# Kernel optimization log

Hardware: AMD Instinct MI355X
Metric: run time of the kernel (lower is better)

## Reference

```python
import math
import jax, jax.numpy as jnp
import numpy as np

B, H, W, CP = 64, 512, 512, 400
HALF_X = W // 2          # int, matches width//2 in the original
HALF_Y = H / 2.0         # float, matches height/2 in the original
NPTS = CP // 2
PI = math.pi


def fix_radians(tt):
    # Faithful translation of: -relu(-(2pi - relu(-tt)), threshold=-2pi) + relu(tt)
    inner = -(2.0 * PI - jnp.maximum(-tt, 0.0))
    thr = jnp.where(inner > -2.0 * PI, inner, 0.0)  # keras relu with threshold=-2pi
    return -thr + jnp.maximum(tt, 0.0)


def half_contour(pred_norm):
    # pred_norm: [B, H, W] in [0, 1]
    pred1st = jnp.round(pred_norm[:, :, :HALF_X])          # [B, H, W/2]
    x1st = jnp.sum(pred1st, axis=2)                        # [B, H] column count per row
    xaux = jnp.clip(x1st, 0.0, 1.0)                        # relu(.., threshold=0, max_value=1)
    ythtop = HALF_Y - jnp.sum(xaux[:, :HALF_X], axis=1)    # [B]
    ythbottom = HALF_Y + jnp.sum(xaux[:, HALF_X:], axis=1) # [B]
    rows = jnp.arange(W, dtype=pred_norm.dtype)[None, :]   # [1, W] (H == W assumed by original)
    # relu(rows - top) + top == max(rows, top); then min with bottom
    y1st = jnp.minimum(jnp.maximum(rows, ythtop[:, None]), ythbottom[:, None])  # [B, W]
    # Original: x1st <- half_x - x1st, then cart2pol(x1st - half_x, y1st - half_y)
    xc = -x1st                                             # [B, H]
    yc = y1st - HALF_Y                                     # [B, W]
    r1st = jnp.sqrt(xc ** 2 + yc ** 2)                     # [B, H]
    tt1st = fix_radians(jnp.arctan2(yc, xc))               # [B, H]

    tt_new = (PI / 2.0) + jnp.arange(NPTS, dtype=pred_norm.dtype) * (PI / NPTS)  # [NPTS]

    # RBF angular smoothing (get_rbf_points), with periodic wraparound copies
    tt_1 = jnp.concatenate([tt1st - 2.0 * PI, tt1st, tt1st + 2.0 * PI], axis=1)  # [B, 3H]
    r_cat = jnp.concatenate([r1st, r1st, r1st], axis=1)                          # [B, 3H]
    d2 = (tt_1[:, :, None] - tt_new[None, None, :]) ** 2                         # [B, 3H, NPTS]
    d2 = jnp.minimum(d2, 1.0)
    wgt = jnp.exp(-100.0 * d2)                                                   # [B, 3H, NPTS]
    wgt = wgt / jnp.sum(wgt, axis=1, keepdims=True)
    r_new = jnp.einsum('bkn,bk->bn', wgt, r_cat)                                 # [B, NPTS]

    x_new = r_new * jnp.cos(tt_new)[None, :] + HALF_X
    y_new = r_new * jnp.sin(tt_new)[None, :] + HALF_Y
    return jnp.stack([x_new, y_new], axis=-1)              # [B, NPTS, 2]


def setup_inputs() -> dict:
    key = jax.random.key(0)
    inputs = jax.random.uniform(key, (B, H, W, 2), dtype=jnp.float32)
    return {"inputs": inputs}


def reference(inputs) -> jnp.ndarray:
    lvc = inputs[:, :, :, -1]                              # [B, H, W]
    mn = jnp.min(lvc, axis=(1, 2), keepdims=True)
    mx = jnp.max(lvc, axis=(1, 2), keepdims=True)
    lvc_norm = (lvc - mn) / (mx - mn)
    c1 = half_contour(lvc_norm)                            # [B, NPTS, 2]
    c2 = half_contour(lvc_norm[:, :, ::-1])                # mirrored half
    c2 = jnp.concatenate([float(H) - c2[:, :, :1], c2[:, :, 1:]], axis=-1)[:, ::-1, :]
    return jnp.concatenate([c1, c2], axis=1)               # [B, CP, 2]
```

## Files before the change

kernel.cpp:

```cpp
#include <hip/hip_runtime.h>
#include <math.h>
#include <float.h>

#define BB 64
#define HH 512
#define WW 512
#define NPTS 200

#define PMIN_OFF 0
#define PMAX_OFF 2048
#define MN_OFF   4096
#define MX_OFF   4160
#define CNT_OFF  4224

__global__ __launch_bounds__(256) void kminmax(const float* __restrict__ in,
                                               float* __restrict__ ws) {
    int bid = blockIdx.x;
    int b   = bid >> 5;
    int c   = bid & 31;
    int t   = threadIdx.x;
    const float4* base = (const float4*)in + (size_t)b * 131072 + (size_t)c * 4096;
    float vmin = FLT_MAX, vmax = -FLT_MAX;
#pragma unroll
    for (int i = 0; i < 16; ++i) {
        float4 v = base[i * 256 + t];
        vmin = fminf(vmin, fminf(v.y, v.w));
        vmax = fmaxf(vmax, fmaxf(v.y, v.w));
    }
    for (int m = 32; m >= 1; m >>= 1) {
        vmin = fminf(vmin, __shfl_xor(vmin, m, 64));
        vmax = fmaxf(vmax, __shfl_xor(vmax, m, 64));
    }
    __shared__ float smin[4], smax[4];
    int wv = t >> 6;
    if ((t & 63) == 0) { smin[wv] = vmin; smax[wv] = vmax; }
    __syncthreads();
    if (t == 0) {
        float a = fminf(fminf(smin[0], smin[1]), fminf(smin[2], smin[3]));
        float z = fmaxf(fmaxf(smax[0], smax[1]), fmaxf(smax[2], smax[3]));
        ws[PMIN_OFF + bid] = a;
        ws[PMAX_OFF + bid] = z;
    }
}

__global__ __launch_bounds__(64) void kminmax2(float* __restrict__ ws) {
    int b = blockIdx.x;
    int i = threadIdx.x & 31;
    float vmin = ws[PMIN_OFF + b * 32 + i];
    float vmax = ws[PMAX_OFF + b * 32 + i];
    for (int m = 16; m >= 1; m >>= 1) {
        vmin = fminf(vmin, __shfl_xor(vmin, m, 64));
        vmax = fmaxf(vmax, __shfl_xor(vmax, m, 64));
    }
    if (threadIdx.x == 0) { ws[MN_OFF + b] = vmin; ws[MX_OFF + b] = vmax; }
}

__global__ __launch_bounds__(256) void kcount(const float* __restrict__ in,
                                              float* __restrict__ ws) {
    int gwave = (blockIdx.x * 256 + threadIdx.x) >> 6;
    int lane  = threadIdx.x & 63;
    int b     = gwave >> 9;
    int row   = gwave & 511;
    float mn = ws[MN_OFF + b];
    float mx = ws[MX_OFF + b];
    float den = mx - mn;
    const float4* base = (const float4*)in + ((size_t)(b * HH + row)) * 256;
    int cl = 0, cr = 0;
#pragma unroll
    for (int i = 0; i < 4; ++i) {
        float4 v = base[i * 64 + lane];
        float t0 = (v.y - mn) / den;
        float t1 = (v.w - mn) / den;
        int c = (int)rintf(t0) + (int)rintf(t1);
        if (i < 2) cl += c; else cr += c;
    }
    for (int m = 32; m >= 1; m >>= 1) {
        cl += __shfl_xor(cl, m, 64);
        cr += __shfl_xor(cr, m, 64);
    }
    if (lane == 0) {
        ws[CNT_OFF + (b * 2 + 0) * 512 + row] = (float)cl;
        ws[CNT_OFF + (b * 2 + 1) * 512 + row] = (float)cr;
    }
}

__global__ __launch_bounds__(256) void kinterp(const float* __restrict__ ws,
                                               float* __restrict__ out) {
    const float TWO_PI_F = 6.28318530717958647692f;
    const float PI_F     = 3.14159265358979323846f;
    int b    = blockIdx.x >> 1;
    int half = blockIdx.x & 1;
    int t    = threadIdx.x;
    const float* cnt = ws + CNT_OFF + (b * 2 + half) * 512;

    __shared__ float s_tt[512];
    __shared__ float s_r[512];
    __shared__ float s_red[12];

    float c0 = cnt[t];
    float c1 = cnt[t + 256];

    int r0 = (c0 >= 1.0f) ? 1 : 0;
    int r1 = (c1 >= 1.0f) ? 1 : 0;
    for (int m = 32; m >= 1; m >>= 1) {
        r0 += __shfl_xor(r0, m, 64);
        r1 += __shfl_xor(r1, m, 64);
    }
    int wv = t >> 6;
    if ((t & 63) == 0) { s_red[wv] = (float)r0; s_red[4 + wv] = (float)r1; }
    __syncthreads();
    float ythtop    = 256.0f - (s_red[0] + s_red[1] + s_red[2] + s_red[3]);
    float ythbottom = 256.0f + (s_red[4] + s_red[5] + s_red[6] + s_red[7]);

    float sumr_local = 0.0f;
#pragma unroll
    for (int j = 0; j < 2; ++j) {
        int   r  = t + j * 256;
        float x1 = (j == 0) ? c0 : c1;
        float y1 = fminf(fmaxf((float)r, ythtop), ythbottom);
        float xc = -x1;
        float yc = y1 - 256.0f;
        float rr = sqrtf(xc * xc + yc * yc);
        float tt;
        if (x1 == 0.0f && yc == 0.0f) {
            tt = PI_F;
        } else {
            tt = atan2f(yc, xc);
            if (tt < 0.0f) tt += TWO_PI_F;
        }
        s_tt[r] = tt;
        s_r[r]  = rr;
        sumr_local += rr;
    }
    float sr = sumr_local;
    for (int m = 32; m >= 1; m >>= 1) sr += __shfl_xor(sr, m, 64);
    if ((t & 63) == 0) s_red[8 + wv] = sr;
    __syncthreads();
    float sumr = s_red[8] + s_red[9] + s_red[10] + s_red[11];

    if (t < NPTS) {
        float ttn = 1.5707963267948966f + (float)t * 0.015707963267948966f;
        float dmin = 1.0f;
        for (int k = 0; k < 512; ++k) {
            float d  = s_tt[k] - ttn;
            float d2 = fminf(d * d, 1.0f);
            dmin = fminf(dmin, d2);
        }
        float num = 0.0f, den = 0.0f;
        for (int k = 0; k < 512; ++k) {
            float d  = s_tt[k] - ttn;
            float d2 = fminf(d * d, 1.0f);
            float w  = __expf(-100.0f * (d2 - dmin));
            den += w;
            num += w * s_r[k];
        }
        float w1 = __expf(-100.0f * (1.0f - dmin));
        den += 1024.0f * w1;
        num += 2.0f * w1 * sumr;

        float rn   = num / den;
        float xnew = rn * cosf(ttn) + 256.0f;
        float ynew = rn * sinf(ttn) + 256.0f;

        if (half == 0) {
            out[((size_t)b * 400 + t) * 2 + 0] = xnew;
            out[((size_t)b * 400 + t) * 2 + 1] = ynew;
        } else {
            int p = 399 - t;
            out[((size_t)b * 400 + p) * 2 + 0] = 512.0f - xnew;
            out[((size_t)b * 400 + p) * 2 + 1] = ynew;
        }
    }
}

extern "C" void kernel_launch(void* const* d_in, const int* in_sizes, int n_in,
                              void* d_out, int out_size, void* d_ws, size_t ws_size,
                              hipStream_t stream) {
    const float* in  = (const float*)d_in[0];
    float*       out = (float*)d_out;
    float*       ws  = (float*)d_ws;

    kminmax <<<dim3(2048), dim3(256), 0, stream>>>(in, ws);
    kminmax2<<<dim3(64),   dim3(64),  0, stream>>>(ws);
    kcount  <<<dim3(8192), dim3(256), 0, stream>>>(in, ws);
    kinterp <<<dim3(128),  dim3(256), 0, stream>>>(ws, out);
}
```

Measured before the change: 228.2 us.

## Parallelize RBF interpolation across waves and fold final min/max into count kernel

Drops the separate min/max finalization kernel by having each count wave reduce the 32 partial min/max values itself. Splits the interpolation kernel into a polar-conversion kernel that writes angles and radii to workspace, and a points kernel that gives each output point its own wave, with lanes sharing the 512 samples and combining results by wave reductions. The old kinterp ran only 128 blocks, each doing serial 512-iteration loops per thread, so it underused the GPU. The change adds an extra launch and workspace round trips in exchange for much wider parallelism in that stage.

Result: faster. 222.3 us (-2.6%).

```diff
diff --git a/kernel.cpp b/kernel.cpp
--- a/kernel.cpp
+++ b/kernel.cpp
@@ -9,9 +9,10 @@
 
 #define PMIN_OFF 0
 #define PMAX_OFF 2048
-#define MN_OFF   4096
-#define MX_OFF   4160
 #define CNT_OFF  4224
+#define TT_OFF   69760
+#define RR_OFF   135296
+#define SUMR_OFF 200832
 
 __global__ __launch_bounds__(256) void kminmax(const float* __restrict__ in,
                                                float* __restrict__ ws) {
@@ -43,27 +44,21 @@
     }
 }
 
-__global__ __launch_bounds__(64) void kminmax2(float* __restrict__ ws) {
-    int b = blockIdx.x;
-    int i = threadIdx.x & 31;
-    float vmin = ws[PMIN_OFF + b * 32 + i];
-    float vmax = ws[PMAX_OFF + b * 32 + i];
-    for (int m = 16; m >= 1; m >>= 1) {
-        vmin = fminf(vmin, __shfl_xor(vmin, m, 64));
-        vmax = fmaxf(vmax, __shfl_xor(vmax, m, 64));
-    }
-    if (threadIdx.x == 0) { ws[MN_OFF + b] = vmin; ws[MX_OFF + b] = vmax; }
-}
-
 __global__ __launch_bounds__(256) void kcount(const float* __restrict__ in,
                                               float* __restrict__ ws) {
     int gwave = (blockIdx.x * 256 + threadIdx.x) >> 6;
     int lane  = threadIdx.x & 63;
     int b     = gwave >> 9;
     int row   = gwave & 511;
-    float mn = ws[MN_OFF + b];
-    float mx = ws[MX_OFF + b];
+
+    float mn = ws[PMIN_OFF + b * 32 + (lane & 31)];
+    float mx = ws[PMAX_OFF + b * 32 + (lane & 31)];
+    for (int m = 16; m >= 1; m >>= 1) {
+        mn = fminf(mn, __shfl_xor(mn, m, 64));
+        mx = fmaxf(mx, __shfl_xor(mx, m, 64));
+    }
     float den = mx - mn;
+
     const float4* base = (const float4*)in + ((size_t)(b * HH + row)) * 256;
     int cl = 0, cr = 0;
 #pragma unroll
@@ -84,17 +79,15 @@
     }
 }
 
-__global__ __launch_bounds__(256) void kinterp(const float* __restrict__ ws,
-                                               float* __restrict__ out) {
+__global__ __launch_bounds__(256) void kpolar(float* __restrict__ ws) {
     const float TWO_PI_F = 6.28318530717958647692f;
     const float PI_F     = 3.14159265358979323846f;
-    int b    = blockIdx.x >> 1;
-    int half = blockIdx.x & 1;
-    int t    = threadIdx.x;
-    const float* cnt = ws + CNT_OFF + (b * 2 + half) * 512;
-
-    __shared__ float s_tt[512];
-    __shared__ float s_r[512];
+    int b2 = blockIdx.x;
+    int t  = threadIdx.x;
+    const float* cnt = ws + CNT_OFF + b2 * 512;
+    float* tt_out    = ws + TT_OFF  + b2 * 512;
+    float* rr_out    = ws + RR_OFF  + b2 * 512;
+
     __shared__ float s_red[12];
 
     float c0 = cnt[t];
@@ -128,40 +121,68 @@
             tt = atan2f(yc, xc);
             if (tt < 0.0f) tt += TWO_PI_F;
         }
-        s_tt[r] = tt;
-        s_r[r]  = rr;
+        tt_out[r] = tt;
+        rr_out[r] = rr;
         sumr_local += rr;
     }
     float sr = sumr_local;
     for (int m = 32; m >= 1; m >>= 1) sr += __shfl_xor(sr, m, 64);
     if ((t & 63) == 0) s_red[8 + wv] = sr;
     __syncthreads();
-    float sumr = s_red[8] + s_red[9] + s_red[10] + s_red[11];
-
-    if (t < NPTS) {
-        float ttn = 1.5707963267948966f + (float)t * 0.015707963267948966f;
-        float dmin = 1.0f;
-        for (int k = 0; k < 512; ++k) {
-            float d  = s_tt[k] - ttn;
-            float d2 = fminf(d * d, 1.0f);
-            dmin = fminf(dmin, d2);
-        }
-        float num = 0.0f, den = 0.0f;
-        for (int k = 0; k < 512; ++k) {
-            float d  = s_tt[k] - ttn;
-            float d2 = fminf(d * d, 1.0f);
-            float w  = __expf(-100.0f * (d2 - dmin));
-            den += w;
-            num += w * s_r[k];
-        }
-        float w1 = __expf(-100.0f * (1.0f - dmin));
-        den += 1024.0f * w1;
-        num += 2.0f * w1 * sumr;
-
-        float rn   = num / den;
-        float xnew = rn * cosf(ttn) + 256.0f;
-        float ynew = rn * sinf(ttn) + 256.0f;
-
+    if (t == 0)
+        ws[SUMR_OFF + b2] = s_red[8] + s_red[9] + s_red[10] + s_red[11];
+}
+
+__global__ __launch_bounds__(256) void kpoints(const float* __restrict__ ws,
+                                               float* __restrict__ out) {
+    int w    = (blockIdx.x * 256 + threadIdx.x) >> 6;
+    int lane = threadIdx.x & 63;
+    int b2   = w / NPTS;
+    int t    = w - b2 * NPTS;
+    int b    = b2 >> 1;
+    int half = b2 & 1;
+
+    const float4* ttv = (const float4*)(ws + TT_OFF + b2 * 512);
+    const float4* rrv = (const float4*)(ws + RR_OFF + b2 * 512);
+    float4 ta = ttv[lane], tb = ttv[lane + 64];
+    float4 ra = rrv[lane], rb = rrv[lane + 64];
+    float tts[8] = {ta.x, ta.y, ta.z, ta.w, tb.x, tb.y, tb.z, tb.w};
+    float rs[8]  = {ra.x, ra.y, ra.z, ra.w, rb.x, rb.y, rb.z, rb.w};
+
+    float ttn = 1.5707963267948966f + (float)t * 0.015707963267948966f;
+
+    float d2[8];
+    float dmin = 1.0f;
+#pragma unroll
+    for (int i = 0; i < 8; ++i) {
+        float d = tts[i] - ttn;
+        d2[i] = fminf(d * d, 1.0f);
+        dmin = fminf(dmin, d2[i]);
+    }
+    for (int m = 32; m >= 1; m >>= 1) dmin = fminf(dmin, __shfl_xor(dmin, m, 64));
+
+    float num = 0.0f, den = 0.0f;
+#pragma unroll
+    for (int i = 0; i < 8; ++i) {
+        float wg = __expf(-100.0f * (d2[i] - dmin));
+        den += wg;
+        num += wg * rs[i];
+    }
+    for (int m = 32; m >= 1; m >>= 1) {
+        den += __shfl_xor(den, m, 64);
+        num += __shfl_xor(num, m, 64);
+    }
+
+    float sumr = ws[SUMR_OFF + b2];
+    float w1 = __expf(-100.0f * (1.0f - dmin));
+    den += 1024.0f * w1;
+    num += 2.0f * w1 * sumr;
+
+    float rn   = num / den;
+    float xnew = rn * cosf(ttn) + 256.0f;
+    float ynew = rn * sinf(ttn) + 256.0f;
+
+    if (lane == 0) {
         if (half == 0) {
             out[((size_t)b * 400 + t) * 2 + 0] = xnew;
             out[((size_t)b * 400 + t) * 2 + 1] = ynew;
@@ -180,8 +201,8 @@
     float*       out = (float*)d_out;
     float*       ws  = (float*)d_ws;
 
-    kminmax <<<dim3(2048), dim3(256), 0, stream>>>(in, ws);
-    kminmax2<<<dim3(64),   dim3(64),  0, stream>>>(ws);
-    kcount  <<<dim3(8192), dim3(256), 0, stream>>>(in, ws);
-    kinterp <<<dim3(128),  dim3(256), 0, stream>>>(ws, out);
-}
+    kminmax<<<dim3(2048), dim3(256), 0, stream>>>(in, ws);
+    kcount <<<dim3(8192), dim3(256), 0, stream>>>(in, ws);
+    kpolar <<<dim3(128),  dim3(256), 0, stream>>>(ws);
+    kpoints<<<dim3(6400), dim3(256), 0, stream>>>(ws, out);
+}
```
